# Kernel tuning notes

Hardware: AMD Instinct MI355X
Metric: run time of the kernel (lower is better)

## Reference

```python
import jax, jax.numpy as jnp
import numpy as np

B, L, F, H = 1024, 256, 128, 256
A, CH, OUT = 128, 256, 512


def setup_inputs() -> dict:
    key = jax.random.key(0)
    ks = jax.random.split(key, 12)
    s = lambda k, shape, fan: (jax.random.normal(k, shape, jnp.float32) / np.float32(np.sqrt(fan)))
    return dict(
        input_batch=jax.random.normal(ks[0], (B, L, F), jnp.float32),
        tte=jax.random.randint(ks[1], (B,), 0, L, jnp.int32),
        W_ih=s(ks[2], (3 * H, F), F), W_hh=s(ks[3], (3 * H, H), H),
        b_ih=jnp.zeros((3 * H,), jnp.float32), b_hh=jnp.zeros((3 * H,), jnp.float32),
        W_out=s(ks[4], (F, H), H), b_out=jnp.zeros((F,), jnp.float32),
        Wa=s(ks[5], (H, A), H), Ua=s(ks[6], (F, A), F), va=s(ks[7], (A,), A),
        W1=s(ks[8], (H + F, CH), H + F), b1=jnp.zeros((CH,), jnp.float32),
        W2=s(ks[9], (CH, OUT), CH), b2=jnp.zeros((OUT,), jnp.float32),
    )


def _gru_step(x, h, W_ih, W_hh, b_ih, b_hh):
    # torch.nn.GRU single-step math, batched over B
    gi = x @ W_ih.T + b_ih          # [B,3H]
    gh = h @ W_hh.T + b_hh          # [B,3H]
    i_r, i_z, i_n = jnp.split(gi, 3, axis=-1)
    h_r, h_z, h_n = jnp.split(gh, 3, axis=-1)
    r = jax.nn.sigmoid(i_r + h_r)
    z = jax.nn.sigmoid(i_z + h_z)
    n = jnp.tanh(i_n + r * h_n)
    return (1.0 - z) * n + z * h


def reference(input_batch, tte, W_ih, W_hh, b_ih, b_hh, W_out, b_out,
              Wa, Ua, va, W1, b1, W2, b2):
    Bn, Ln, Fn = input_batch.shape
    Hn = W_hh.shape[1]
    h0 = jnp.zeros((Bn, Hn), input_batch.dtype)
    xs = jnp.moveaxis(input_batch, 1, 0)  # [L,B,F]
    ts = jnp.arange(Ln)

    def step(h, inp):
        x_t, t = inp
        h_new = _gru_step(x_t, h, W_ih, W_hh, b_ih, b_hh)
        active = (t < tte)[:, None]          # ragged length mask [B,1]
        h = jnp.where(active, h_new, h)      # freeze state past tte
        out_t = jnp.where(active, h_new @ W_out.T + b_out, 0.0)
        hid_t = jnp.where(active, h_new, 0.0)
        return h, (out_t, hid_t)

    _, (outs, hids) = jax.lax.scan(step, h0, (xs, ts))
    output_batch = jnp.moveaxis(outs, 0, 1)   # [B,L,F], zero-padded like the torch code
    hidden_vec = jnp.moveaxis(hids, 0, 1)     # [B,L,H], zero-padded

    # last measurement at index tte (the torch code indexes batch[tte])
    last = jnp.take_along_axis(input_batch, tte[:, None, None].astype(jnp.int32), axis=1)[:, 0]  # [B,F]

    # decoder: additive attention over the full padded trajectory
    scores = jnp.tanh(hidden_vec @ Wa + (last @ Ua)[:, None, :]) @ va   # [B,L]
    alpha = jax.nn.softmax(scores, axis=-1)
    context = jnp.einsum('bl,blh->bh', alpha, hidden_vec)               # [B,H]

    # causes network: MLP + softmax over cause x time-bin grid
    zc = jax.nn.relu(jnp.concatenate([context, last], axis=-1) @ W1 + b1)
    fht = jax.nn.softmax(zc @ W2 + b2, axis=-1)                         # [B,OUT]
    return output_batch, fht
```

## Files before the change

kernel.cpp:

```cpp
#include <hip/hip_runtime.h>

#define B_ 1024
#define L_ 256
#define F_ 128
#define H_ 256

typedef __bf16 bf16x8 __attribute__((ext_vector_type(8)));
typedef __bf16 bf16x4 __attribute__((ext_vector_type(4)));
typedef float f32x4 __attribute__((ext_vector_type(4)));
typedef int i32x4 __attribute__((ext_vector_type(4)));

#define MFMA16(a, b, c) __builtin_amdgcn_mfma_f32_16x16x32_bf16((a), (b), (c), 0, 0, 0)
#define MFMA_I8(a, b, c) __builtin_amdgcn_mfma_i32_16x16x64_i8((a), (b), (c), 0, 0, 0)
#define BAR_LDS() asm volatile("s_waitcnt lgkmcnt(0)\n\ts_barrier" ::: "memory")

__device__ __forceinline__ float rcp_f(float x) { return __builtin_amdgcn_rcpf(x); }
__device__ __forceinline__ float sigm(float x) { return rcp_f(1.f + __expf(-x)); }
__device__ __forceinline__ float tanh_f(float x) {
  float ax = fabsf(x);
  float e = __expf(-2.f * ax);
  float r = (1.f - e) * rcp_f(1.f + e);
  return copysignf(r, x);
}
__device__ __forceinline__ bf16x8 ld8(const __bf16* p) { return *(const bf16x8*)p; }
__device__ __forceinline__ float wave_max(float v) {
#pragma unroll
  for (int d = 1; d < 64; d <<= 1) v = fmaxf(v, __shfl_xor(v, d));
  return v;
}
__device__ __forceinline__ float wave_sum(float v) {
#pragma unroll
  for (int d = 1; d < 64; d <<= 1) v += __shfl_xor(v, d);
  return v;
}
__device__ __forceinline__ unsigned pack4(float a, float b, float c, float d, float inv) {
  return (unsigned)(unsigned char)(signed char)__float2int_rn(a * inv)
       | ((unsigned)(unsigned char)(signed char)__float2int_rn(b * inv) << 8)
       | ((unsigned)(unsigned char)(signed char)__float2int_rn(c * inv) << 16)
       | ((unsigned)(unsigned char)(signed char)__float2int_rn(d * inv) << 24);
}

__global__ void cvt_kernel(const float* __restrict__ wih_f, const float* __restrict__ wa_f,
                           const float* __restrict__ ua_f, const float* __restrict__ w1_f,
                           const float* __restrict__ w2_f,
                           __bf16* __restrict__ wih, __bf16* __restrict__ wa_t,
                           __bf16* __restrict__ ua_t, __bf16* __restrict__ w1_t,
                           __bf16* __restrict__ w2_t) {
  int i = blockIdx.x * 256 + threadIdx.x;
  if (i < 98304) wih[i] = (__bf16)wih_f[i];
  else if (i < 131072) {
    int j = i - 98304; int a = j >> 8, k = j & 255;
    wa_t[j] = (__bf16)wa_f[k * 128 + a];
  } else if (i < 147456) {
    int j = i - 131072; int a = j >> 7, f = j & 127;
    ua_t[j] = (__bf16)ua_f[f * 128 + a];
  } else if (i < 245760) {
    int j = i - 147456; int c = j / 384, k = j - c * 384;
    w1_t[j] = (__bf16)w1_f[k * 256 + c];
  } else if (i < 376832) {
    int j = i - 245760; int o = j >> 8, k = j & 255;
    w2_t[j] = (__bf16)w2_f[k * 512 + o];
  }
}

__global__ void quant_kernel(const float* __restrict__ whh_f, const float* __restrict__ wout_f,
                             signed char* __restrict__ wqg_f,
                             signed char* __restrict__ wqo_f,
                             float* __restrict__ dq) {
  const int c = blockIdx.x * 256 + threadIdx.x;
  if (c >= 896) return;
  const float* row = (c < 768) ? whh_f + (size_t)c * 256 : wout_f + (size_t)(c - 768) * 256;
  float m = 0.f;
  for (int k4 = 0; k4 < 64; ++k4) {
    float4 v = *(const float4*)(row + k4 * 4);
    m = fmaxf(m, fmaxf(fmaxf(fabsf(v.x), fabsf(v.y)), fmaxf(fabsf(v.z), fabsf(v.w))));
  }
  const float inv = (m > 1e-30f) ? 127.f / m : 0.f;
  dq[c] = m / 16129.f;
  if (c < 768) {
    const int g = c >> 8, cc = c & 255;
    const int t16 = cc >> 4, l15q = cc & 15;
    for (int kt = 0; kt < 4; ++kt)
      for (int lgq = 0; lgq < 4; ++lgq) {
        signed char* dst = wqg_f + (size_t)((((g * 16 + t16) * 4 + kt) * 64) + lgq * 16 + l15q) * 16;
        const float* src = row + kt * 64 + lgq * 16;
        for (int j4 = 0; j4 < 4; ++j4) {
          float4 v = *(const float4*)(src + j4 * 4);
          *(unsigned*)(dst + j4 * 4) = pack4(v.x, v.y, v.z, v.w, inv);
        }
      }
  } else {
    const int oc = c - 768;
    const int t8 = oc >> 4, l15q = oc & 15;
    for (int kt = 0; kt < 4; ++kt)
      for (int lgq = 0; lgq < 4; ++lgq) {
        signed char* dst = wqo_f + (size_t)(((t8 * 4 + kt) * 64) + lgq * 16 + l15q) * 16;
        const float* src = row + kt * 64 + lgq * 16;
        for (int j4 = 0; j4 < 4; ++j4) {
          float4 v = *(const float4*)(src + j4 * 4);
          *(unsigned*)(dst + j4 * 4) = pack4(v.x, v.y, v.z, v.w, inv);
        }
      }
  }
}

__global__ __launch_bounds__(512, 2) void gi_gemm_kernel(
    const float* __restrict__ x, const float* __restrict__ b_ih,
    const float* __restrict__ b_hh, const __bf16* __restrict__ wih,
    const int* __restrict__ tte, __bf16* __restrict__ gi,
    float* __restrict__ out) {
  const int tid = threadIdx.x;
  const int lane = tid & 63, w = tid >> 6;
  const int l15 = lane & 15, lg = lane >> 4, kofs = lg * 8;
  const int bblk = blockIdx.x & 63, tgrp = blockIdx.x >> 6;
  const int b0 = bblk * 16;

  {
    const int pr = tid >> 1, ph = tid & 1;
    const int bl = pr >> 4, tl = pr & 15;
    const int bb = b0 + bl, tt = tgrp * 16 + tl;
    if (tt >= tte[bb]) {
      float4* dst = (float4*)(out + ((size_t)bb * L_ + tt) * F_) + ph * 16;
#pragma unroll
      for (int i = 0; i < 16; ++i) dst[i] = float4{0.f, 0.f, 0.f, 0.f};
    }
  }

  int tmaxB = 0;
  for (int i = 0; i < 16; ++i) tmaxB = max(tmaxB, tte[b0 + i]);
  if (tgrp * 16 > tmaxB) return;

  bf16x8 wf[6][4];
  float bias[6];
#pragma unroll
  for (int tile = 0; tile < 6; ++tile) {
    const int gate = tile >> 1;
    const int c = w * 32 + (tile & 1) * 16 + l15;
    const int col = gate * 256 + c;
#pragma unroll
    for (int kt = 0; kt < 4; ++kt) wf[tile][kt] = ld8(wih + (size_t)col * 128 + kt * 32 + kofs);
    bias[tile] = (gate == 0) ? b_ih[c] + b_hh[c]
               : (gate == 1) ? b_ih[256 + c] + b_hh[256 + c]
                             : b_ih[512 + c];
  }

#pragma unroll 1
  for (int ti = 0; ti < 16; ++ti) {
    const int t = tgrp * 16 + ti;
    if (t > tmaxB) break;
    const float* xb = x + ((size_t)(b0 + l15) * L_ + t) * F_ + kofs;
    bf16x8 xfr[4];
#pragma unroll
    for (int kt = 0; kt < 4; ++kt) {
      float4 a = *(const float4*)(xb + kt * 32);
      float4 b = *(const float4*)(xb + kt * 32 + 4);
      xfr[kt][0] = (__bf16)a.x; xfr[kt][1] = (__bf16)a.y;
      xfr[kt][2] = (__bf16)a.z; xfr[kt][3] = (__bf16)a.w;
      xfr[kt][4] = (__bf16)b.x; xfr[kt][5] = (__bf16)b.y;
      xfr[kt][6] = (__bf16)b.z; xfr[kt][7] = (__bf16)b.w;
    }
    f32x4 acc[6];
#pragma unroll
    for (int tile = 0; tile < 6; ++tile) {
      acc[tile][0] = bias[tile]; acc[tile][1] = bias[tile];
      acc[tile][2] = bias[tile]; acc[tile][3] = bias[tile];
    }
#pragma unroll
    for (int kt = 0; kt < 4; ++kt)
#pragma unroll
      for (int tile = 0; tile < 6; ++tile)
        acc[tile] = MFMA16(xfr[kt], wf[tile][kt], acc[tile]);

    const size_t chunk = (((size_t)t * 64 + bblk) * 8 + w) * 6;
#pragma unroll
    for (int tile = 0; tile < 6; ++tile) {
      bf16x4 pk;
      pk[0] = (__bf16)acc[tile][0]; pk[1] = (__bf16)acc[tile][1];
      pk[2] = (__bf16)acc[tile][2]; pk[3] = (__bf16)acc[tile][3];
      *(bf16x4*)(gi + (chunk + tile) * 256 + (lg * 16 + l15) * 4) = pk;
    }
  }
}

__global__ __launch_bounds__(1024) void gru256_kernel(
    const int* __restrict__ tte, const float* __restrict__ b_hh,
    const signed char* __restrict__ wqg_f, const signed char* __restrict__ wqo_f,
    const float* __restrict__ dq, const __bf16* __restrict__ gi,
    const float* __restrict__ b_out,
    __bf16* __restrict__ hid, float* __restrict__ out) {
  __shared__ signed char hb[2][4][288];
  const int tid = threadIdx.x;
  const int lane = tid & 63, w = tid >> 6;
  const int l15 = lane & 15, lg = lane >> 4;
  const int blk = blockIdx.x;
  const int b0 = blk * 4;

  for (int i = tid; i < 2 * 4 * 288; i += 1024) ((signed char*)hb)[i] = 0;

  i32x4 wR[4], wZ[4], wN[4];
#pragma unroll
  for (int kt = 0; kt < 4; ++kt) {
    wR[kt] = *(const i32x4*)(wqg_f + (size_t)((((0 * 16 + w) * 4 + kt) * 64) + lane) * 16);
    wZ[kt] = *(const i32x4*)(wqg_f + (size_t)((((1 * 16 + w) * 4 + kt) * 64) + lane) * 16);
    wN[kt] = *(const i32x4*)(wqg_f + (size_t)((((2 * 16 + w) * 4 + kt) * 64) + lane) * 16);
  }
  const int ocol = (w & 7) * 16 + l15;
  i32x4 ow[4];
#pragma unroll
  for (int kt = 0; kt < 4; ++kt)
    ow[kt] = *(const i32x4*)(wqo_f + (size_t)(((w & 7) * 4 + kt) * 64 + lane) * 16);
  const float dqo = dq[768 + ocol];
  const float bo = b_out[ocol];
  int tteO[4];
#pragma unroll
  for (int r = 0; r < 4; ++r) tteO[r] = tte[b0 + r];
  float* outp = out + ((size_t)b0 * L_) * F_ + ocol;

  const int groww = lane >> 4, gcolw = w * 16 + (lane & 15);
  const float dqR = dq[gcolw], dqZ = dq[256 + gcolw], dqN = dq[512 + gcolw];
  const float bhn = b_hh[512 + gcolw];
  const int tteL = tte[b0 + groww];
  int tmax = 0;
#pragma unroll
  for (int i = 0; i < 4; ++i) tmax = max(tmax, tte[b0 + i]);

  const size_t gb0 = (((size_t)(blk >> 2) * 8 + (gcolw >> 5)) * 6 + ((gcolw >> 4) & 1)) * 256
                   + (size_t)((blk & 3) * 16 + (gcolw & 15)) * 4 + groww;
  const __bf16* gp = gi + gb0;
  __bf16 gRn = gp[0], gZn = gp[512], gNn = gp[1024];
  const __bf16* gpp = gp + 786432;

  __bf16* hidp = hid + ((size_t)(b0 + groww) * L_) * H_ + gcolw;
  float hprev = 0.f;

  __syncthreads();

#pragma unroll 1
  for (int t = 0; t < tmax; ++t) {
    const int c = t & 1, nc = c ^ 1;

    const float grf = (float)gRn, gzf = (float)gZn, gnf = (float)gNn;
    gRn = gpp[0]; gZn = gpp[512]; gNn = gpp[1024];
    if (t < 254) gpp += 786432;

    i32x4 aR = {0, 0, 0, 0}, aZ = {0, 0, 0, 0}, aN = {0, 0, 0, 0}, ac = {0, 0, 0, 0};
#pragma unroll
    for (int kt = 0; kt < 4; ++kt) {
      const i32x4 hA = *(const i32x4*)&hb[c][l15 & 3][kt * 64 + lg * 16];
      aR = MFMA_I8(hA, wR[kt], aR);
      aZ = MFMA_I8(hA, wZ[kt], aZ);
      aN = MFMA_I8(hA, wN[kt], aN);
      if (w < 8) ac = MFMA_I8(hA, ow[kt], ac);
    }
    if (w < 8 && t > 0) {
      if (lg == 0) {
#pragma unroll
        for (int r = 0; r < 4; ++r)
          if (t - 1 < tteO[r]) outp[(size_t)r * (L_ * F_)] = (float)ac[r] * dqo + bo;
      }
      outp += F_;
    }

    {
      const int srcl = lane & 15;
      int tR0 = __shfl(aR[0], srcl), tR1 = __shfl(aR[1], srcl);
      int tR2 = __shfl(aR[2], srcl), tR3 = __shfl(aR[3], srcl);
      int tZ0 = __shfl(aZ[0], srcl), tZ1 = __shfl(aZ[1], srcl);
      int tZ2 = __shfl(aZ[2], srcl), tZ3 = __shfl(aZ[3], srcl);
      int tN0 = __shfl(aN[0], srcl), tN1 = __shfl(aN[1], srcl);
      int tN2 = __shfl(aN[2], srcl), tN3 = __shfl(aN[3], srcl);
      const int vR = groww == 0 ? tR0 : groww == 1 ? tR1 : groww == 2 ? tR2 : tR3;
      const int vZ = groww == 0 ? tZ0 : groww == 1 ? tZ1 : groww == 2 ? tZ2 : tZ3;
      const int vN = groww == 0 ? tN0 : groww == 1 ? tN1 : groww == 2 ? tN2 : tN3;

      const float rg = sigm(grf + (float)vR * dqR);
      const float zg = sigm(gzf + (float)vZ * dqZ);
      const float ng = tanh_f(gnf + rg * ((float)vN * dqN + bhn));
      const float hnew = zg * (hprev - ng) + ng;
      const float hw = (t < tteL) ? hnew : hprev;
      hprev = hw;
      hb[nc][groww][gcolw] = (signed char)__float2int_rn(hw * 127.f);
      if (t < tteL) *hidp = (__bf16)hw;
      hidp += H_;
    }
    BAR_LDS();
  }

  if (w < 8 && tmax > 0) {
    const int cf = tmax & 1;
    i32x4 ac = {0, 0, 0, 0};
#pragma unroll
    for (int kt = 0; kt < 4; ++kt) {
      const i32x4 hA = *(const i32x4*)&hb[cf][l15 & 3][kt * 64 + lg * 16];
      ac = MFMA_I8(hA, ow[kt], ac);
    }
    if (lg == 0) {
#pragma unroll
      for (int r = 0; r < 4; ++r)
        if (tmax - 1 < tteO[r]) outp[(size_t)r * (L_ * F_)] = (float)ac[r] * dqo + bo;
    }
  }
}

__global__ __launch_bounds__(512, 2) void decoder3_kernel(
    const float* __restrict__ x, const int* __restrict__ tte,
    const __bf16* __restrict__ hid, const __bf16* __restrict__ wa_t,
    const __bf16* __restrict__ ua_t, const __bf16* __restrict__ w1_t,
    const __bf16* __restrict__ w2_t, const float* __restrict__ va,
    const float* __restrict__ b1, const float* __restrict__ b2,
    float* __restrict__ fht) {
  __shared__ __bf16 catb[16][392];
  __shared__ float u_s[4][128];
  __shared__ float sa[4][256];
  __shared__ __bf16 z1b[16][264];
  __shared__ float lg2[4][516];
  __shared__ float ctxp[2][4][256];
  __shared__ float va_s[128];
  __shared__ int tte_s[4];
  const int tid = threadIdx.x;
  const int lane = tid & 63, w = tid >> 6;
  const int l15 = lane & 15, lg = lane >> 4, kofs = lg * 8;
  const int b0 = blockIdx.x * 4;

  if (tid < 4) tte_s[tid] = tte[b0 + tid];
  if (tid < 128) va_s[tid] = va[tid];
  if (tid < 392)
    for (int r = 4; r < 16; ++r) catb[r][tid] = (__bf16)0.f;
  if (tid < 264)
    for (int r = 4; r < 16; ++r) z1b[r][tid] = (__bf16)0.f;
  __syncthreads();

  {
    const int row = tid >> 7, c = tid & 127;
    catb[row][256 + c] = (__bf16)x[((size_t)(b0 + row) * L_ + tte_s[row]) * F_ + c];
  }
  __syncthreads();

  {
    f32x4 uacc = {0, 0, 0, 0};
#pragma unroll
    for (int kt = 0; kt < 4; ++kt) {
      const bf16x8 af = *(const bf16x8*)&catb[l15][256 + kt * 32 + kofs];
      const bf16x8 bf = ld8(ua_t + (size_t)(w * 16 + l15) * 128 + kt * 32 + kofs);
      uacc = MFMA16(af, bf, uacc);
    }
#pragma unroll
    for (int r = 0; r < 4; ++r) {
      const int row = 4 * lg + r;
      if (row < 4) u_s[row][w * 16 + l15] = uacc[r];
    }
  }
  __syncthreads();

  bf16x8 zero8;
#pragma unroll
  for (int j = 0; j < 8; ++j) zero8[j] = (__bf16)0.f;
#pragma unroll 1
  for (int it = 0; it < 8; ++it) {
    const int pair = it * 8 + w;
    const int b = pair >> 4, mtile = pair & 15;
    const int tteB = tte_s[b];
    const int trow = mtile * 16 + l15;
    const __bf16* hrow = hid + ((size_t)(b0 + b) * L_ + trow) * H_ + kofs;
    bf16x8 af[8];
#pragma unroll
    for (int kt = 0; kt < 8; ++kt) af[kt] = (trow < tteB) ? ld8(hrow + kt * 32) : zero8;
    f32x4 sacc[8];
#pragma unroll
    for (int ct = 0; ct < 8; ++ct) { sacc[ct][0] = 0; sacc[ct][1] = 0; sacc[ct][2] = 0; sacc[ct][3] = 0; }
#pragma unroll
    for (int kt = 0; kt < 8; ++kt)
#pragma unroll
      for (int ct = 0; ct < 8; ++ct)
        sacc[ct] = MFMA16(af[kt], ld8(wa_t + (size_t)(ct * 16 + l15) * 256 + kt * 32 + kofs), sacc[ct]);
    float sp[4] = {0, 0, 0, 0};
#pragma unroll
    for (int ct = 0; ct < 8; ++ct) {
      const int a = ct * 16 + l15;
      const float ua = u_s[b][a], vv = va_s[a];
#pragma unroll
      for (int r = 0; r < 4; ++r) sp[r] += tanh_f(sacc[ct][r] + ua) * vv;
    }
#pragma unroll
    for (int r = 0; r < 4; ++r) {
      sp[r] += __shfl_xor(sp[r], 1);
      sp[r] += __shfl_xor(sp[r], 2);
      sp[r] += __shfl_xor(sp[r], 4);
      sp[r] += __shfl_xor(sp[r], 8);
    }
    if (l15 == 0) {
#pragma unroll
      for (int r = 0; r < 4; ++r) sa[b][mtile * 16 + 4 * lg + r] = sp[r];
    }
  }
  __syncthreads();

  if (w < 4) {
    float sv[4];
#pragma unroll
    for (int j = 0; j < 4; ++j) sv[j] = sa[w][lane + 64 * j];
    float mx = fmaxf(fmaxf(sv[0], sv[1]), fmaxf(sv[2], sv[3]));
    mx = wave_max(mx);
    float es[4], ss = 0.f;
#pragma unroll
    for (int j = 0; j < 4; ++j) { es[j] = __expf(sv[j] - mx); ss += es[j]; }
    ss = wave_sum(ss);
    const float inv = rcp_f(ss);
#pragma unroll
    for (int j = 0; j < 4; ++j) sa[w][lane + 64 * j] = es[j] * inv;
  }
  __syncthreads();

  {
    const int be = w & 3, half = w >> 2;
    const int tteE = tte_s[be];
    float c4[4] = {0.f, 0.f, 0.f, 0.f};
    const __bf16* hp = hid + ((size_t)(b0 + be) * L_ + half) * H_ + lane * 4;
#pragma unroll 2
    for (int t = half; t < tteE; t += 2) {
      const float al = sa[be][t];
      const bf16x4 hv = *(const bf16x4*)hp;
      hp += 2 * H_;
#pragma unroll
      for (int j = 0; j < 4; ++j) c4[j] += al * (float)hv[j];
    }
#pragma unroll
    for (int j = 0; j < 4; ++j) ctxp[half][be][lane * 4 + j] = c4[j];
  }
  __syncthreads();
  if (w < 4) {
#pragma unroll
    for (int j = 0; j < 4; ++j)
      catb[w][lane * 4 + j] = (__bf16)(ctxp[0][w][lane * 4 + j] + ctxp[1][w][lane * 4 + j]);
  }
  __syncthreads();

#pragma unroll 1
  for (int half = 0; half < 2; ++half) {
    const int nt = w * 2 + half;
    f32x4 zacc = {0, 0, 0, 0};
#pragma unroll
    for (int kt = 0; kt < 12; ++kt) {
      const bf16x8 af = *(const bf16x8*)&catb[l15][kt * 32 + kofs];
      const bf16x8 bf = ld8(w1_t + (size_t)(nt * 16 + l15) * 384 + kt * 32 + kofs);
      zacc = MFMA16(af, bf, zacc);
    }
    const float bb = b1[nt * 16 + l15];
#pragma unroll
    for (int r = 0; r < 4; ++r) {
      const int row = 4 * lg + r;
      if (row < 4) z1b[row][nt * 16 + l15] = (__bf16)fmaxf(zacc[r] + bb, 0.f);
    }
  }
  __syncthreads();

#pragma unroll 1
  for (int q = 0; q < 4; ++q) {
    const int nt = w * 4 + q;
    f32x4 oacc = {0, 0, 0, 0};
#pragma unroll
    for (int kt = 0; kt < 8; ++kt) {
      const bf16x8 af = *(const bf16x8*)&z1b[l15][kt * 32 + kofs];
      const bf16x8 bf = ld8(w2_t + (size_t)(nt * 16 + l15) * 256 + kt * 32 + kofs);
      oacc = MFMA16(af, bf, oacc);
    }
    const float bb = b2[nt * 16 + l15];
#pragma unroll
    for (int r = 0; r < 4; ++r) {
      const int row = 4 * lg + r;
      if (row < 4) lg2[row][nt * 16 + l15] = oacc[r] + bb;
    }
  }
  __syncthreads();
  if (w < 4) {
    float lv[8];
    float mx = -1e30f;
#pragma unroll
    for (int j = 0; j < 8; ++j) { lv[j] = lg2[w][lane + 64 * j]; mx = fmaxf(mx, lv[j]); }
    mx = wave_max(mx);
    float s2 = 0.f;
#pragma unroll
    for (int j = 0; j < 8; ++j) { lv[j] = __expf(lv[j] - mx); s2 += lv[j]; }
    s2 = wave_sum(s2);
    const float inv2 = rcp_f(s2);
#pragma unroll
    for (int j = 0; j < 8; ++j)
      fht[(size_t)(b0 + w) * 512 + lane + 64 * j] = lv[j] * inv2;
  }
}

extern "C" void kernel_launch(void* const* d_in, const int* in_sizes, int n_in,
                              void* d_out, int out_size, void* d_ws, size_t ws_size,
                              hipStream_t stream) {
  const float* x = (const float*)d_in[0];
  const int* tte = (const int*)d_in[1];
  const float* W_ih = (const float*)d_in[2];
  const float* W_hh = (const float*)d_in[3];
  const float* b_ih = (const float*)d_in[4];
  const float* b_hh = (const float*)d_in[5];
  const float* W_out = (const float*)d_in[6];
  const float* b_out = (const float*)d_in[7];
  const float* Wa = (const float*)d_in[8];
  const float* Ua = (const float*)d_in[9];
  const float* va = (const float*)d_in[10];
  const float* W1 = (const float*)d_in[11];
  const float* b1 = (const float*)d_in[12];
  const float* W2 = (const float*)d_in[13];
  const float* b2 = (const float*)d_in[14];

  char* ws = (char*)d_ws;
  __bf16* wih = (__bf16*)(ws + 0);
  __bf16* wa_t = (__bf16*)(ws + 196608);
  __bf16* ua_t = (__bf16*)(ws + 262144);
  __bf16* w1_t = (__bf16*)(ws + 294912);
  __bf16* w2_t = (__bf16*)(ws + 491520);
  signed char* wqg_f = (signed char*)(ws + 753664);
  signed char* wqo_f = (signed char*)(ws + 950272);
  float* dq = (float*)(ws + 983040);
  __bf16* hid = (__bf16*)(ws + 1048576);
  __bf16* gi = (__bf16*)(ws + 135266304);

  float* out = (float*)d_out;
  float* fht = out + (size_t)33554432;

  cvt_kernel<<<1472, 256, 0, stream>>>(W_ih, Wa, Ua, W1, W2,
                                       wih, wa_t, ua_t, w1_t, w2_t);
  quant_kernel<<<4, 256, 0, stream>>>(W_hh, W_out, wqg_f, wqo_f, dq);
  gi_gemm_kernel<<<1024, 512, 0, stream>>>(x, b_ih, b_hh, wih, tte, gi, out);
  gru256_kernel<<<256, 1024, 0, stream>>>(tte, b_hh, wqg_f, wqo_f, dq, gi,
                                          b_out, hid, out);
  decoder3_kernel<<<256, 512, 0, stream>>>(x, tte, hid, wa_t, ua_t, w1_t, w2_t,
                                           va, b1, b2, fht);
}
```

Baseline: 711.5 us.

## Fuse GRU and decoder into one kernel with per-group flag handoff

Merges the cvt and quant weight-prep kernels into a single launch and folds the GRU recurrence and the attention/MLP decoder into one kernel. Blocks 0-255 run the recurrence and publish a per-group release flag when they finish. Blocks 256-511 spin on that flag and then run the decoder, so decoding of early-finishing groups overlaps the still-running recurrences and a launch gap disappears. The risks are decoder blocks occupying CUs while they spin, possible deadlock if not all blocks are co-resident (a guard counter bounds the spin), the larger 1024-thread decoder block with half its waves idle, and an extra memset launch to clear the flags.

```diff
diff --git a/kernel.cpp b/kernel.cpp
--- a/kernel.cpp
+++ b/kernel.cpp
@@ -40,34 +40,34 @@
        | ((unsigned)(unsigned char)(signed char)__float2int_rn(d * inv) << 24);
 }
 
-__global__ void cvt_kernel(const float* __restrict__ wih_f, const float* __restrict__ wa_f,
-                           const float* __restrict__ ua_f, const float* __restrict__ w1_f,
-                           const float* __restrict__ w2_f,
-                           __bf16* __restrict__ wih, __bf16* __restrict__ wa_t,
-                           __bf16* __restrict__ ua_t, __bf16* __restrict__ w1_t,
-                           __bf16* __restrict__ w2_t) {
-  int i = blockIdx.x * 256 + threadIdx.x;
-  if (i < 98304) wih[i] = (__bf16)wih_f[i];
-  else if (i < 131072) {
-    int j = i - 98304; int a = j >> 8, k = j & 255;
-    wa_t[j] = (__bf16)wa_f[k * 128 + a];
-  } else if (i < 147456) {
-    int j = i - 131072; int a = j >> 7, f = j & 127;
-    ua_t[j] = (__bf16)ua_f[f * 128 + a];
-  } else if (i < 245760) {
-    int j = i - 147456; int c = j / 384, k = j - c * 384;
-    w1_t[j] = (__bf16)w1_f[k * 256 + c];
-  } else if (i < 376832) {
-    int j = i - 245760; int o = j >> 8, k = j & 255;
-    w2_t[j] = (__bf16)w2_f[k * 512 + o];
-  }
-}
-
-__global__ void quant_kernel(const float* __restrict__ whh_f, const float* __restrict__ wout_f,
-                             signed char* __restrict__ wqg_f,
-                             signed char* __restrict__ wqo_f,
-                             float* __restrict__ dq) {
-  const int c = blockIdx.x * 256 + threadIdx.x;
+__global__ void prep_kernel(const float* __restrict__ wih_f, const float* __restrict__ wa_f,
+                            const float* __restrict__ ua_f, const float* __restrict__ w1_f,
+                            const float* __restrict__ w2_f, const float* __restrict__ whh_f,
+                            const float* __restrict__ wout_f,
+                            __bf16* __restrict__ wih, __bf16* __restrict__ wa_t,
+                            __bf16* __restrict__ ua_t, __bf16* __restrict__ w1_t,
+                            __bf16* __restrict__ w2_t,
+                            signed char* __restrict__ wqg_f, signed char* __restrict__ wqo_f,
+                            float* __restrict__ dq) {
+  if (blockIdx.x < 1472) {
+    int i = blockIdx.x * 256 + threadIdx.x;
+    if (i < 98304) wih[i] = (__bf16)wih_f[i];
+    else if (i < 131072) {
+      int j = i - 98304; int a = j >> 8, k = j & 255;
+      wa_t[j] = (__bf16)wa_f[k * 128 + a];
+    } else if (i < 147456) {
+      int j = i - 131072; int a = j >> 7, f = j & 127;
+      ua_t[j] = (__bf16)ua_f[f * 128 + a];
+    } else if (i < 245760) {
+      int j = i - 147456; int c = j / 384, k = j - c * 384;
+      w1_t[j] = (__bf16)w1_f[k * 256 + c];
+    } else if (i < 376832) {
+      int j = i - 245760; int o = j >> 8, k = j & 255;
+      w2_t[j] = (__bf16)w2_f[k * 512 + o];
+    }
+    return;
+  }
+  const int c = (blockIdx.x - 1472) * 256 + threadIdx.x;
   if (c >= 896) return;
   const float* row = (c < 768) ? whh_f + (size_t)c * 256 : wout_f + (size_t)(c - 768) * 256;
   float m = 0.f;
@@ -182,133 +182,19 @@
   }
 }
 
-__global__ __launch_bounds__(1024) void gru256_kernel(
-    const int* __restrict__ tte, const float* __restrict__ b_hh,
+__global__ __launch_bounds__(1024) void mega_kernel(
+    const float* __restrict__ x, const int* __restrict__ tte,
+    const float* __restrict__ b_hh,
     const signed char* __restrict__ wqg_f, const signed char* __restrict__ wqo_f,
     const float* __restrict__ dq, const __bf16* __restrict__ gi,
     const float* __restrict__ b_out,
-    __bf16* __restrict__ hid, float* __restrict__ out) {
+    const __bf16* __restrict__ wa_t, const __bf16* __restrict__ ua_t,
+    const __bf16* __restrict__ w1_t, const __bf16* __restrict__ w2_t,
+    const float* __restrict__ va, const float* __restrict__ b1,
+    const float* __restrict__ b2,
+    __bf16* __restrict__ hid, float* __restrict__ out, float* __restrict__ fht,
+    int* __restrict__ flags) {
   __shared__ signed char hb[2][4][288];
-  const int tid = threadIdx.x;
-  const int lane = tid & 63, w = tid >> 6;
-  const int l15 = lane & 15, lg = lane >> 4;
-  const int blk = blockIdx.x;
-  const int b0 = blk * 4;
-
-  for (int i = tid; i < 2 * 4 * 288; i += 1024) ((signed char*)hb)[i] = 0;
-
-  i32x4 wR[4], wZ[4], wN[4];
-#pragma unroll
-  for (int kt = 0; kt < 4; ++kt) {
-    wR[kt] = *(const i32x4*)(wqg_f + (size_t)((((0 * 16 + w) * 4 + kt) * 64) + lane) * 16);
-    wZ[kt] = *(const i32x4*)(wqg_f + (size_t)((((1 * 16 + w) * 4 + kt) * 64) + lane) * 16);
-    wN[kt] = *(const i32x4*)(wqg_f + (size_t)((((2 * 16 + w) * 4 + kt) * 64) + lane) * 16);
-  }
-  const int ocol = (w & 7) * 16 + l15;
-  i32x4 ow[4];
-#pragma unroll
-  for (int kt = 0; kt < 4; ++kt)
-    ow[kt] = *(const i32x4*)(wqo_f + (size_t)(((w & 7) * 4 + kt) * 64 + lane) * 16);
-  const float dqo = dq[768 + ocol];
-  const float bo = b_out[ocol];
-  int tteO[4];
-#pragma unroll
-  for (int r = 0; r < 4; ++r) tteO[r] = tte[b0 + r];
-  float* outp = out + ((size_t)b0 * L_) * F_ + ocol;
-
-  const int groww = lane >> 4, gcolw = w * 16 + (lane & 15);
-  const float dqR = dq[gcolw], dqZ = dq[256 + gcolw], dqN = dq[512 + gcolw];
-  const float bhn = b_hh[512 + gcolw];
-  const int tteL = tte[b0 + groww];
-  int tmax = 0;
-#pragma unroll
-  for (int i = 0; i < 4; ++i) tmax = max(tmax, tte[b0 + i]);
-
-  const size_t gb0 = (((size_t)(blk >> 2) * 8 + (gcolw >> 5)) * 6 + ((gcolw >> 4) & 1)) * 256
-                   + (size_t)((blk & 3) * 16 + (gcolw & 15)) * 4 + groww;
-  const __bf16* gp = gi + gb0;
-  __bf16 gRn = gp[0], gZn = gp[512], gNn = gp[1024];
-  const __bf16* gpp = gp + 786432;
-
-  __bf16* hidp = hid + ((size_t)(b0 + groww) * L_) * H_ + gcolw;
-  float hprev = 0.f;
-
-  __syncthreads();
-
-#pragma unroll 1
-  for (int t = 0; t < tmax; ++t) {
-    const int c = t & 1, nc = c ^ 1;
-
-    const float grf = (float)gRn, gzf = (float)gZn, gnf = (float)gNn;
-    gRn = gpp[0]; gZn = gpp[512]; gNn = gpp[1024];
-    if (t < 254) gpp += 786432;
-
-    i32x4 aR = {0, 0, 0, 0}, aZ = {0, 0, 0, 0}, aN = {0, 0, 0, 0}, ac = {0, 0, 0, 0};
-#pragma unroll
-    for (int kt = 0; kt < 4; ++kt) {
-      const i32x4 hA = *(const i32x4*)&hb[c][l15 & 3][kt * 64 + lg * 16];
-      aR = MFMA_I8(hA, wR[kt], aR);
-      aZ = MFMA_I8(hA, wZ[kt], aZ);
-      aN = MFMA_I8(hA, wN[kt], aN);
-      if (w < 8) ac = MFMA_I8(hA, ow[kt], ac);
-    }
-    if (w < 8 && t > 0) {
-      if (lg == 0) {
-#pragma unroll
-        for (int r = 0; r < 4; ++r)
-          if (t - 1 < tteO[r]) outp[(size_t)r * (L_ * F_)] = (float)ac[r] * dqo + bo;
-      }
-      outp += F_;
-    }
-
-    {
-      const int srcl = lane & 15;
-      int tR0 = __shfl(aR[0], srcl), tR1 = __shfl(aR[1], srcl);
-      int tR2 = __shfl(aR[2], srcl), tR3 = __shfl(aR[3], srcl);
-      int tZ0 = __shfl(aZ[0], srcl), tZ1 = __shfl(aZ[1], srcl);
-      int tZ2 = __shfl(aZ[2], srcl), tZ3 = __shfl(aZ[3], srcl);
-      int tN0 = __shfl(aN[0], srcl), tN1 = __shfl(aN[1], srcl);
-      int tN2 = __shfl(aN[2], srcl), tN3 = __shfl(aN[3], srcl);
-      const int vR = groww == 0 ? tR0 : groww == 1 ? tR1 : groww == 2 ? tR2 : tR3;
-      const int vZ = groww == 0 ? tZ0 : groww == 1 ? tZ1 : groww == 2 ? tZ2 : tZ3;
-      const int vN = groww == 0 ? tN0 : groww == 1 ? tN1 : groww == 2 ? tN2 : tN3;
-
-      const float rg = sigm(grf + (float)vR * dqR);
-      const float zg = sigm(gzf + (float)vZ * dqZ);
-      const float ng = tanh_f(gnf + rg * ((float)vN * dqN + bhn));
-      const float hnew = zg * (hprev - ng) + ng;
-      const float hw = (t < tteL) ? hnew : hprev;
-      hprev = hw;
-      hb[nc][groww][gcolw] = (signed char)__float2int_rn(hw * 127.f);
-      if (t < tteL) *hidp = (__bf16)hw;
-      hidp += H_;
-    }
-    BAR_LDS();
-  }
-
-  if (w < 8 && tmax > 0) {
-    const int cf = tmax & 1;
-    i32x4 ac = {0, 0, 0, 0};
-#pragma unroll
-    for (int kt = 0; kt < 4; ++kt) {
-      const i32x4 hA = *(const i32x4*)&hb[cf][l15 & 3][kt * 64 + lg * 16];
-      ac = MFMA_I8(hA, ow[kt], ac);
-    }
-    if (lg == 0) {
-#pragma unroll
-      for (int r = 0; r < 4; ++r)
-        if (tmax - 1 < tteO[r]) outp[(size_t)r * (L_ * F_)] = (float)ac[r] * dqo + bo;
-    }
-  }
-}
-
-__global__ __launch_bounds__(512, 2) void decoder3_kernel(
-    const float* __restrict__ x, const int* __restrict__ tte,
-    const __bf16* __restrict__ hid, const __bf16* __restrict__ wa_t,
-    const __bf16* __restrict__ ua_t, const __bf16* __restrict__ w1_t,
-    const __bf16* __restrict__ w2_t, const float* __restrict__ va,
-    const float* __restrict__ b1, const float* __restrict__ b2,
-    float* __restrict__ fht) {
   __shared__ __bf16 catb[16][392];
   __shared__ float u_s[4][128];
   __shared__ float sa[4][256];
@@ -317,10 +203,136 @@
   __shared__ float ctxp[2][4][256];
   __shared__ float va_s[128];
   __shared__ int tte_s[4];
+
   const int tid = threadIdx.x;
   const int lane = tid & 63, w = tid >> 6;
   const int l15 = lane & 15, lg = lane >> 4, kofs = lg * 8;
-  const int b0 = blockIdx.x * 4;
+
+  if (blockIdx.x < 256) {
+    const int blk = blockIdx.x;
+    const int b0 = blk * 4;
+
+    for (int i = tid; i < 2 * 4 * 288; i += 1024) ((signed char*)hb)[i] = 0;
+
+    i32x4 wR[4], wZ[4], wN[4];
+#pragma unroll
+    for (int kt = 0; kt < 4; ++kt) {
+      wR[kt] = *(const i32x4*)(wqg_f + (size_t)((((0 * 16 + w) * 4 + kt) * 64) + lane) * 16);
+      wZ[kt] = *(const i32x4*)(wqg_f + (size_t)((((1 * 16 + w) * 4 + kt) * 64) + lane) * 16);
+      wN[kt] = *(const i32x4*)(wqg_f + (size_t)((((2 * 16 + w) * 4 + kt) * 64) + lane) * 16);
+    }
+    const int ocol = (w & 7) * 16 + l15;
+    i32x4 ow[4];
+#pragma unroll
+    for (int kt = 0; kt < 4; ++kt)
+      ow[kt] = *(const i32x4*)(wqo_f + (size_t)(((w & 7) * 4 + kt) * 64 + lane) * 16);
+    const float dqo = dq[768 + ocol];
+    const float bo = b_out[ocol];
+    int tteO[4];
+#pragma unroll
+    for (int r = 0; r < 4; ++r) tteO[r] = tte[b0 + r];
+    float* outp = out + ((size_t)b0 * L_) * F_ + ocol;
+
+    const int groww = lane >> 4, gcolw = w * 16 + (lane & 15);
+    const float dqR = dq[gcolw], dqZ = dq[256 + gcolw], dqN = dq[512 + gcolw];
+    const float bhn = b_hh[512 + gcolw];
+    const int tteL = tte[b0 + groww];
+    int tmax = 0;
+#pragma unroll
+    for (int i = 0; i < 4; ++i) tmax = max(tmax, tte[b0 + i]);
+
+    const size_t gb0 = (((size_t)(blk >> 2) * 8 + (gcolw >> 5)) * 6 + ((gcolw >> 4) & 1)) * 256
+                     + (size_t)((blk & 3) * 16 + (gcolw & 15)) * 4 + groww;
+    const __bf16* gp = gi + gb0;
+    __bf16 gRn = gp[0], gZn = gp[512], gNn = gp[1024];
+    const __bf16* gpp = gp + 786432;
+
+    __bf16* hidp = hid + ((size_t)(b0 + groww) * L_) * H_ + gcolw;
+    float hprev = 0.f;
+
+    __syncthreads();
+
+#pragma unroll 1
+    for (int t = 0; t < tmax; ++t) {
+      const int c = t & 1, nc = c ^ 1;
+
+      const float grf = (float)gRn, gzf = (float)gZn, gnf = (float)gNn;
+      gRn = gpp[0]; gZn = gpp[512]; gNn = gpp[1024];
+      if (t < 254) gpp += 786432;
+
+      i32x4 aR = {0, 0, 0, 0}, aZ = {0, 0, 0, 0}, aN = {0, 0, 0, 0}, ac = {0, 0, 0, 0};
+#pragma unroll
+      for (int kt = 0; kt < 4; ++kt) {
+        const i32x4 hA = *(const i32x4*)&hb[c][l15 & 3][kt * 64 + lg * 16];
+        aR = MFMA_I8(hA, wR[kt], aR);
+        aZ = MFMA_I8(hA, wZ[kt], aZ);
+        aN = MFMA_I8(hA, wN[kt], aN);
+        if (w < 8) ac = MFMA_I8(hA, ow[kt], ac);
+      }
+      if (w < 8 && t > 0) {
+        if (lg == 0) {
+#pragma unroll
+          for (int r = 0; r < 4; ++r)
+            if (t - 1 < tteO[r]) outp[(size_t)r * (L_ * F_)] = (float)ac[r] * dqo + bo;
+        }
+        outp += F_;
+      }
+
+      {
+        const int srcl = lane & 15;
+        int tR0 = __shfl(aR[0], srcl), tR1 = __shfl(aR[1], srcl);
+        int tR2 = __shfl(aR[2], srcl), tR3 = __shfl(aR[3], srcl);
+        int tZ0 = __shfl(aZ[0], srcl), tZ1 = __shfl(aZ[1], srcl);
+        int tZ2 = __shfl(aZ[2], srcl), tZ3 = __shfl(aZ[3], srcl);
+        int tN0 = __shfl(aN[0], srcl), tN1 = __shfl(aN[1], srcl);
+        int tN2 = __shfl(aN[2], srcl), tN3 = __shfl(aN[3], srcl);
+        const int vR = groww == 0 ? tR0 : groww == 1 ? tR1 : groww == 2 ? tR2 : tR3;
+        const int vZ = groww == 0 ? tZ0 : groww == 1 ? tZ1 : groww == 2 ? tZ2 : tZ3;
+        const int vN = groww == 0 ? tN0 : groww == 1 ? tN1 : groww == 2 ? tN2 : tN3;
+
+        const float rg = sigm(grf + (float)vR * dqR);
+        const float zg = sigm(gzf + (float)vZ * dqZ);
+        const float ng = tanh_f(gnf + rg * ((float)vN * dqN + bhn));
+        const float hnew = zg * (hprev - ng) + ng;
+        const float hw = (t < tteL) ? hnew : hprev;
+        hprev = hw;
+        hb[nc][groww][gcolw] = (signed char)__float2int_rn(hw * 127.f);
+        if (t < tteL) *hidp = (__bf16)hw;
+        hidp += H_;
+      }
+      BAR_LDS();
+    }
+
+    if (w < 8 && tmax > 0) {
+      const int cf = tmax & 1;
+      i32x4 ac = {0, 0, 0, 0};
+#pragma unroll
+      for (int kt = 0; kt < 4; ++kt) {
+        const i32x4 hA = *(const i32x4*)&hb[cf][l15 & 3][kt * 64 + lg * 16];
+        ac = MFMA_I8(hA, ow[kt], ac);
+      }
+      if (lg == 0) {
+#pragma unroll
+        for (int r = 0; r < 4; ++r)
+          if (tmax - 1 < tteO[r]) outp[(size_t)r * (L_ * F_)] = (float)ac[r] * dqo + bo;
+      }
+    }
+
+    __syncthreads();
+    if (tid == 0)
+      __hip_atomic_store(&flags[blk], 1, __ATOMIC_RELEASE, __HIP_MEMORY_SCOPE_AGENT);
+    return;
+  }
+
+  const int grp = blockIdx.x - 256;
+  const int b0 = grp * 4;
+
+  if (tid == 0) {
+    long guard = 0;
+    while (__hip_atomic_load(&flags[grp], __ATOMIC_ACQUIRE, __HIP_MEMORY_SCOPE_AGENT) == 0)
+      if (++guard > 300000000L) break;
+  }
+  __syncthreads();
 
   if (tid < 4) tte_s[tid] = tte[b0 + tid];
   if (tid < 128) va_s[tid] = va[tid];
@@ -330,13 +342,13 @@
     for (int r = 4; r < 16; ++r) z1b[r][tid] = (__bf16)0.f;
   __syncthreads();
 
-  {
+  if (tid < 512) {
     const int row = tid >> 7, c = tid & 127;
     catb[row][256 + c] = (__bf16)x[((size_t)(b0 + row) * L_ + tte_s[row]) * F_ + c];
   }
   __syncthreads();
 
-  {
+  if (w < 8) {
     f32x4 uacc = {0, 0, 0, 0};
 #pragma unroll
     for (int kt = 0; kt < 4; ++kt) {
@@ -352,45 +364,47 @@
   }
   __syncthreads();
 
-  bf16x8 zero8;
-#pragma unroll
-  for (int j = 0; j < 8; ++j) zero8[j] = (__bf16)0.f;
+  if (w < 8) {
+    bf16x8 zero8;
+#pragma unroll
+    for (int j = 0; j < 8; ++j) zero8[j] = (__bf16)0.f;
 #pragma unroll 1
-  for (int it = 0; it < 8; ++it) {
-    const int pair = it * 8 + w;
-    const int b = pair >> 4, mtile = pair & 15;
-    const int tteB = tte_s[b];
-    const int trow = mtile * 16 + l15;
-    const __bf16* hrow = hid + ((size_t)(b0 + b) * L_ + trow) * H_ + kofs;
-    bf16x8 af[8];
-#pragma unroll
-    for (int kt = 0; kt < 8; ++kt) af[kt] = (trow < tteB) ? ld8(hrow + kt * 32) : zero8;
-    f32x4 sacc[8];
-#pragma unroll
-    for (int ct = 0; ct < 8; ++ct) { sacc[ct][0] = 0; sacc[ct][1] = 0; sacc[ct][2] = 0; sacc[ct][3] = 0; }
-#pragma unroll
-    for (int kt = 0; kt < 8; ++kt)
-#pragma unroll
-      for (int ct = 0; ct < 8; ++ct)
-        sacc[ct] = MFMA16(af[kt], ld8(wa_t + (size_t)(ct * 16 + l15) * 256 + kt * 32 + kofs), sacc[ct]);
-    float sp[4] = {0, 0, 0, 0};
-#pragma unroll
-    for (int ct = 0; ct < 8; ++ct) {
-      const int a = ct * 16 + l15;
-      const float ua = u_s[b][a], vv = va_s[a];
-#pragma unroll
-      for (int r = 0; r < 4; ++r) sp[r] += tanh_f(sacc[ct][r] + ua) * vv;
-    }
-#pragma unroll
-    for (int r = 0; r < 4; ++r) {
-      sp[r] += __shfl_xor(sp[r], 1);
-      sp[r] += __shfl_xor(sp[r], 2);
-      sp[r] += __shfl_xor(sp[r], 4);
-      sp[r] += __shfl_xor(sp[r], 8);
-    }
-    if (l15 == 0) {
-#pragma unroll
-      for (int r = 0; r < 4; ++r) sa[b][mtile * 16 + 4 * lg + r] = sp[r];
+    for (int it = 0; it < 8; ++it) {
+      const int pair = it * 8 + w;
+      const int b = pair >> 4, mtile = pair & 15;
+      const int tteB = tte_s[b];
+      const int trow = mtile * 16 + l15;
+      const __bf16* hrow = hid + ((size_t)(b0 + b) * L_ + trow) * H_ + kofs;
+      bf16x8 af[8];
+#pragma unroll
+      for (int kt = 0; kt < 8; ++kt) af[kt] = (trow < tteB) ? ld8(hrow + kt * 32) : zero8;
+      f32x4 sacc[8];
+#pragma unroll
+      for (int ct = 0; ct < 8; ++ct) { sacc[ct][0] = 0; sacc[ct][1] = 0; sacc[ct][2] = 0; sacc[ct][3] = 0; }
+#pragma unroll
+      for (int kt = 0; kt < 8; ++kt)
+#pragma unroll
+        for (int ct = 0; ct < 8; ++ct)
+          sacc[ct] = MFMA16(af[kt], ld8(wa_t + (size_t)(ct * 16 + l15) * 256 + kt * 32 + kofs), sacc[ct]);
+      float sp[4] = {0, 0, 0, 0};
+#pragma unroll
+      for (int ct = 0; ct < 8; ++ct) {
+        const int a = ct * 16 + l15;
+        const float ua = u_s[b][a], vv = va_s[a];
+#pragma unroll
+        for (int r = 0; r < 4; ++r) sp[r] += tanh_f(sacc[ct][r] + ua) * vv;
+      }
+#pragma unroll
+      for (int r = 0; r < 4; ++r) {
+        sp[r] += __shfl_xor(sp[r], 1);
+        sp[r] += __shfl_xor(sp[r], 2);
+        sp[r] += __shfl_xor(sp[r], 4);
+        sp[r] += __shfl_xor(sp[r], 8);
+      }
+      if (l15 == 0) {
+#pragma unroll
+        for (int r = 0; r < 4; ++r) sa[b][mtile * 16 + 4 * lg + r] = sp[r];
+      }
     }
   }
   __syncthreads();
@@ -411,7 +425,7 @@
   }
   __syncthreads();
 
-  {
+  if (w < 8) {
     const int be = w & 3, half = w >> 2;
     const int tteE = tte_s[be];
     float c4[4] = {0.f, 0.f, 0.f, 0.f};
@@ -435,40 +449,44 @@
   }
   __syncthreads();
 
+  if (w < 8) {
 #pragma unroll 1
-  for (int half = 0; half < 2; ++half) {
-    const int nt = w * 2 + half;
-    f32x4 zacc = {0, 0, 0, 0};
-#pragma unroll
-    for (int kt = 0; kt < 12; ++kt) {
-      const bf16x8 af = *(const bf16x8*)&catb[l15][kt * 32 + kofs];
-      const bf16x8 bf = ld8(w1_t + (size_t)(nt * 16 + l15) * 384 + kt * 32 + kofs);
-      zacc = MFMA16(af, bf, zacc);
-    }
-    const float bb = b1[nt * 16 + l15];
-#pragma unroll
-    for (int r = 0; r < 4; ++r) {
-      const int row = 4 * lg + r;
-      if (row < 4) z1b[row][nt * 16 + l15] = (__bf16)fmaxf(zacc[r] + bb, 0.f);
-    }
-  }
-  __syncthreads();
-
+    for (int half = 0; half < 2; ++half) {
+      const int nt = w * 2 + half;
+      f32x4 zacc = {0, 0, 0, 0};
+#pragma unroll
+      for (int kt = 0; kt < 12; ++kt) {
+        const bf16x8 af = *(const bf16x8*)&catb[l15][kt * 32 + kofs];
+        const bf16x8 bf = ld8(w1_t + (size_t)(nt * 16 + l15) * 384 + kt * 32 + kofs);
+        zacc = MFMA16(af, bf, zacc);
+      }
+      const float bb = b1[nt * 16 + l15];
+#pragma unroll
+      for (int r = 0; r < 4; ++r) {
+        const int row = 4 * lg + r;
+        if (row < 4) z1b[row][nt * 16 + l15] = (__bf16)fmaxf(zacc[r] + bb, 0.f);
+      }
+    }
+  }
+  __syncthreads();
+
+  if (w < 8) {
 #pragma unroll 1
-  for (int q = 0; q < 4; ++q) {
-    const int nt = w * 4 + q;
-    f32x4 oacc = {0, 0, 0, 0};
-#pragma unroll
-    for (int kt = 0; kt < 8; ++kt) {
-      const bf16x8 af = *(const bf16x8*)&z1b[l15][kt * 32 + kofs];
-      const bf16x8 bf = ld8(w2_t + (size_t)(nt * 16 + l15) * 256 + kt * 32 + kofs);
-      oacc = MFMA16(af, bf, oacc);
-    }
-    const float bb = b2[nt * 16 + l15];
-#pragma unroll
-    for (int r = 0; r < 4; ++r) {
-      const int row = 4 * lg + r;
-      if (row < 4) lg2[row][nt * 16 + l15] = oacc[r] + bb;
+    for (int q = 0; q < 4; ++q) {
+      const int nt = w * 4 + q;
+      f32x4 oacc = {0, 0, 0, 0};
+#pragma unroll
+      for (int kt = 0; kt < 8; ++kt) {
+        const bf16x8 af = *(const bf16x8*)&z1b[l15][kt * 32 + kofs];
+        const bf16x8 bf = ld8(w2_t + (size_t)(nt * 16 + l15) * 256 + kt * 32 + kofs);
+        oacc = MFMA16(af, bf, oacc);
+      }
+      const float bb = b2[nt * 16 + l15];
+#pragma unroll
+      for (int r = 0; r < 4; ++r) {
+        const int row = 4 * lg + r;
+        if (row < 4) lg2[row][nt * 16 + l15] = oacc[r] + bb;
+      }
     }
   }
   __syncthreads();
@@ -517,18 +535,19 @@
   signed char* wqg_f = (signed char*)(ws + 753664);
   signed char* wqo_f = (signed char*)(ws + 950272);
   float* dq = (float*)(ws + 983040);
+  int* flags = (int*)(ws + 987136);
   __bf16* hid = (__bf16*)(ws + 1048576);
   __bf16* gi = (__bf16*)(ws + 135266304);
 
   float* out = (float*)d_out;
   float* fht = out + (size_t)33554432;
 
-  cvt_kernel<<<1472, 256, 0, stream>>>(W_ih, Wa, Ua, W1, W2,
-                                       wih, wa_t, ua_t, w1_t, w2_t);
-  quant_kernel<<<4, 256, 0, stream>>>(W_hh, W_out, wqg_f, wqo_f, dq);
+  hipMemsetAsync(flags, 0, 1024, stream);
+  prep_kernel<<<1476, 256, 0, stream>>>(W_ih, Wa, Ua, W1, W2, W_hh, W_out,
+                                        wih, wa_t, ua_t, w1_t, w2_t,
+                                        wqg_f, wqo_f, dq);
   gi_gemm_kernel<<<1024, 512, 0, stream>>>(x, b_ih, b_hh, wih, tte, gi, out);
-  gru256_kernel<<<256, 1024, 0, stream>>>(tte, b_hh, wqg_f, wqo_f, dq, gi,
-                                          b_out, hid, out);
-  decoder3_kernel<<<256, 512, 0, stream>>>(x, tte, hid, wa_t, ua_t, w1_t, w2_t,
-                                           va, b1, b2, fht);
-}
+  mega_kernel<<<512, 1024, 0, stream>>>(x, tte, b_hh, wqg_f, wqo_f, dq, gi,
+                                        b_out, wa_t, ua_t, w1_t, w2_t, va, b1, b2,
+                                        hid, out, fht, flags);
+}
```

Result: slower. 814.1 us (+14.4%).
